# Kernel tuning notes

Hardware: AMD Instinct MI355X
Metric: run time of the kernel (lower is better)

## Reference

```python
import jax, jax.numpy as jnp
import numpy as np
from jax import lax


def setup_inputs() -> dict:
    key = jax.random.key(0)
    k1, k2 = jax.random.split(key)
    x = jax.random.normal(k1, (16, 256, 64, 64), dtype=jnp.float32)
    weight = jax.random.normal(k2, (1024, 256), dtype=jnp.float32)  # codebook (K, C)
    return {"x": x, "weight": weight}


def reference(x, weight):
    B, C, H, W = x.shape
    # (b c h w) -> (b h w) c
    xf = jnp.transpose(x, (0, 2, 3, 1)).reshape(-1, C)  # [N, C]
    d = (jnp.sum(xf * xf, axis=1, keepdims=True)
         + jnp.sum(weight * weight, axis=1)
         - 2.0 * (xf @ weight.T))
    indices = jnp.argmin(d, axis=1)  # [N], int
    z = weight[indices]  # [N, C] embedding lookup
    codebook_loss = jnp.mean((z - lax.stop_gradient(xf)) ** 2)
    commitment_loss = jnp.mean((xf - lax.stop_gradient(z)) ** 2)
    # straight-through estimator
    zq = xf + lax.stop_gradient(z - xf)
    zq = zq.reshape(B, H, W, C).transpose(0, 3, 1, 2)  # back to [B, C, H, W]
    sequence = indices.reshape(B, H, W)
    return zq, sequence, codebook_loss, commitment_loss
```

## Files before the change

kernel.cpp:

```cpp
#include <hip/hip_runtime.h>
#include <cfloat>

#define B_   16
#define C_   256
#define K_   1024
#define HW_  4096
#define N_   (B_ * HW_)
#define CHW_ (C_ * HW_)

#define SEQ_OFF  (B_ * C_ * HW_)
#define LOSS_OFF (SEQ_OFF + N_)

#define WT_F    0
#define WN_F    262144
#define WHB_F   263168
#define WLB_F   394240
#define RLIST_F 525312
#define RCNT_F  590848

#define EPS_GAP 0.03125f

typedef short bf16x8 __attribute__((ext_vector_type(8)));
typedef float f32x16 __attribute__((ext_vector_type(16)));

__device__ __forceinline__ unsigned short bf16_rne(float f) {
    unsigned u = __float_as_uint(f);
    unsigned r = u + 0x7fffu + ((u >> 16) & 1u);
    return (unsigned short)(r >> 16);
}
__device__ __forceinline__ float bf16_to_f(unsigned short h) {
    return __uint_as_float(((unsigned)h) << 16);
}

__global__ __launch_bounds__(256) void transpose_w_kernel(
    const float* __restrict__ w, float* __restrict__ w_t)
{
    const int tid = blockIdx.x * 256 + threadIdx.x;
    const float4 v = reinterpret_cast<const float4*>(w)[tid];
    const int k = tid >> 6;
    const int c = (tid & 63) * 4;
    w_t[(size_t)(c + 0) * K_ + k] = v.x;
    w_t[(size_t)(c + 1) * K_ + k] = v.y;
    w_t[(size_t)(c + 2) * K_ + k] = v.z;
    w_t[(size_t)(c + 3) * K_ + k] = v.w;
}

__global__ __launch_bounds__(256) void wnorm_kernel(
    const float* __restrict__ w, float* __restrict__ wn)
{
    const int k = blockIdx.x * 256 + threadIdx.x;
    const float4* wr = reinterpret_cast<const float4*>(w + (size_t)k * C_);
    float s = 0.f;
#pragma unroll 8
    for (int c4 = 0; c4 < C_ / 4; ++c4) {
        const float4 v = wr[c4];
        s += v.x * v.x + v.y * v.y + v.z * v.z + v.w * v.w;
    }
    wn[k] = s;
}

__global__ __launch_bounds__(256) void wsplit_frag_kernel(
    const float* __restrict__ w, unsigned short* __restrict__ whb,
    unsigned short* __restrict__ wlb)
{
    const int tid = blockIdx.x * 256 + threadIdx.x;
    const int k  = tid >> 5;
    const int c8 = tid & 31;
    const float* src = w + (size_t)k * C_ + c8 * 8;
    unsigned short h[8], lo[8];
#pragma unroll
    for (int j = 0; j < 8; ++j) {
        const float v = src[j];
        h[j] = bf16_rne(v);
        lo[j] = bf16_rne(v - bf16_to_f(h[j]));
    }
    const size_t dst = (size_t)(k >> 5) * 8192 + (size_t)c8 * 256 + (size_t)(k & 31) * 8;
#pragma unroll
    for (int j = 0; j < 8; ++j) { whb[dst + j] = h[j]; wlb[dst + j] = lo[j]; }
}

__global__ __launch_bounds__(256, 2) void argmin_mfma_kernel(
    const float* __restrict__ x, const unsigned short* __restrict__ whb,
    const unsigned short* __restrict__ wlb, const float* __restrict__ wnorm,
    float* __restrict__ seq, int* __restrict__ rlist, int* __restrict__ rcount)
{
    __shared__ __align__(16) char lds[65536];
    const int t  = threadIdx.x;
    const int l  = t & 63;
    const int wv = t >> 6;
    const int nb = blockIdx.x;
    const int b  = nb >> 5;
    const int hw0 = (nb & 31) << 7;
    const float* xb = x + (size_t)b * CHW_ + hw0;

    const int col   = l & 31;
    const int khalf = l >> 5;

    bf16x8 ah[16], al[16];
    {
        float* xs = (float*)lds;
#pragma unroll
        for (int cc = 0; cc < 8; ++cc) {
#pragma unroll
            for (int q = 0; q < 4; ++q) {
                const int fi = q * 256 + t;
                const int cl = fi >> 5;
                const int r4 = (fi & 31) << 2;
                const float4 v = *reinterpret_cast<const float4*>(
                    xb + (size_t)(cc * 32 + cl) * HW_ + r4);
                *reinterpret_cast<float4*>(xs + cl * 132 + r4) = v;
            }
            __syncthreads();
            const int row = wv * 32 + col;
#pragma unroll
            for (int h = 0; h < 2; ++h) {
                const int ks = cc * 2 + h;
                bf16x8 vh, vl;
#pragma unroll
                for (int j = 0; j < 8; ++j) {
                    const float v = xs[(h * 16 + khalf * 8 + j) * 132 + row];
                    const unsigned short hi = bf16_rne(v);
                    vh[j] = (short)hi;
                    vl[j] = (short)bf16_rne(v - bf16_to_f(hi));
                }
                ah[ks] = vh;
                al[ks] = vl;
            }
            __syncthreads();
        }
    }

    char* const buf0 = lds;
    char* const buf1 = lds + 32768;
    const char* whbB = (const char*)whb;
    const char* wlbB = (const char*)wlb;

#define STAGE_CHUNK(ch, dst)                                                        \
    {                                                                               \
        const size_t goff = (size_t)(ch) * 16384 + (size_t)(wv * 4) * 1024;         \
        const int    loff = wv * 4 * 1024;                                          \
        _Pragma("unroll")                                                           \
        for (int rr = 0; rr < 4; ++rr) {                                            \
            __builtin_amdgcn_global_load_lds(                                       \
                (const __attribute__((address_space(1))) void*)                    \
                    (whbB + goff + rr * 1024 + l * 16),                             \
                (__attribute__((address_space(3))) void*)                           \
                    ((dst) + loff + rr * 1024), 16, 0, 0);                          \
            __builtin_amdgcn_global_load_lds(                                       \
                (const __attribute__((address_space(1))) void*)                    \
                    (wlbB + goff + rr * 1024 + l * 16),                             \
                (__attribute__((address_space(3))) void*)                           \
                    ((dst) + 16384 + loff + rr * 1024), 16, 0, 0);                  \
        }                                                                           \
    }

    STAGE_CHUNK(0, buf0);
    __syncthreads();

    float m1v[16], m2v[16];
    int   i1v[16];
#pragma unroll
    for (int r = 0; r < 16; ++r) { m1v[r] = FLT_MAX; m2v[r] = FLT_MAX; i1v[r] = 0; }

    for (int ch = 0; ch < 32; ++ch) {
        char* const curbuf = (ch & 1) ? buf1 : buf0;
        if (ch < 31) { STAGE_CHUNK(ch + 1, (ch & 1) ? buf0 : buf1); }
        const int k0 = ch * 32;
        const float wnc = wnorm[k0 + col];

        f32x16 accA = {0.f}, accB = {0.f};
#pragma unroll
        for (int r = 0; r < 16; ++r) { accA[r] = 0.f; accB[r] = 0.f; }

        const char* hb = curbuf;
        const char* lb = curbuf + 16384;
#pragma unroll
        for (int ks = 0; ks < 16; ++ks) {
            const bf16x8 bh = *reinterpret_cast<const bf16x8*>(hb + ks * 1024 + (l << 4));
            const bf16x8 bl = *reinterpret_cast<const bf16x8*>(lb + ks * 1024 + (l << 4));
            accA = __builtin_amdgcn_mfma_f32_32x32x16_bf16(ah[ks], bh, accA, 0, 0, 0);
            accB = __builtin_amdgcn_mfma_f32_32x32x16_bf16(al[ks], bh, accB, 0, 0, 0);
            accA = __builtin_amdgcn_mfma_f32_32x32x16_bf16(ah[ks], bl, accA, 0, 0, 0);
        }

        const int kidx = k0 + col;
#pragma unroll
        for (int r = 0; r < 16; ++r) {
            const float d = fmaf(-2.f, accA[r] + accB[r], wnc);
            const bool lt = d < m1v[r];
            m2v[r] = lt ? m1v[r] : fminf(m2v[r], d);
            i1v[r] = lt ? kidx : i1v[r];
            m1v[r] = lt ? d : m1v[r];
        }
        __syncthreads();
    }
#undef STAGE_CHUNK

#pragma unroll
    for (int mask = 1; mask <= 16; mask <<= 1) {
#pragma unroll
        for (int r = 0; r < 16; ++r) {
            const float om1 = __shfl_xor(m1v[r], mask, 64);
            const int   oi1 = __shfl_xor(i1v[r], mask, 64);
            const float om2 = __shfl_xor(m2v[r], mask, 64);
            const bool lt = om1 < m1v[r] || (om1 == m1v[r] && oi1 < i1v[r]);
            const float nm2 = lt ? fminf(m1v[r], om2) : fminf(m2v[r], om1);
            i1v[r] = lt ? oi1 : i1v[r];
            m1v[r] = lt ? om1 : m1v[r];
            m2v[r] = nm2;
        }
    }

    if (col == 0) {
#pragma unroll
        for (int r = 0; r < 16; ++r) {
            const int row_local = (r & 3) + 8 * (r >> 2) + 4 * khalf;
            const int n = b * HW_ + hw0 + wv * 32 + row_local;
            seq[n] = (float)i1v[r];
            if (m2v[r] - m1v[r] < EPS_GAP) {
                const int pos = atomicAdd(rcount, 1);
                rlist[pos] = n;
            }
        }
    }
}

__global__ __launch_bounds__(256) void rescue_kernel(
    const float* __restrict__ x, const float* __restrict__ w_t,
    const float* __restrict__ wnorm, const int* __restrict__ rlist,
    const int* __restrict__ rcount, float* __restrict__ seq)
{
    __shared__ float xr[C_];
    __shared__ float bvs[4];
    __shared__ int   bis[4];
    const int t = threadIdx.x;
    const int cnt = *rcount;
    for (int ii = blockIdx.x; ii < cnt; ii += gridDim.x) {
        const int n = rlist[ii];
        const int b = n >> 12, hw = n & 4095;
        xr[t] = x[(size_t)b * CHW_ + (size_t)t * HW_ + hw];
        __syncthreads();
        float best = FLT_MAX; int bidx = 0;
#pragma unroll
        for (int q = 0; q < 4; ++q) {
            const int k = t + q * 256;
            float acc = 0.f;
            for (int c = 0; c < C_; ++c) acc = fmaf(xr[c], w_t[(size_t)c * K_ + k], acc);
            const float d = wnorm[k] - 2.f * acc;
            if (d < best || (d == best && k < bidx)) { best = d; bidx = k; }
        }
#pragma unroll
        for (int mask = 1; mask < 64; mask <<= 1) {
            const float ov = __shfl_xor(best, mask, 64);
            const int   oi = __shfl_xor(bidx, mask, 64);
            if (ov < best || (ov == best && oi < bidx)) { best = ov; bidx = oi; }
        }
        if ((t & 63) == 0) { bvs[t >> 6] = best; bis[t >> 6] = bidx; }
        __syncthreads();
        if (t == 0) {
            float bv = bvs[0]; int bi = bis[0];
#pragma unroll
            for (int w2 = 1; w2 < 4; ++w2)
                if (bvs[w2] < bv || (bvs[w2] == bv && bis[w2] < bi)) { bv = bvs[w2]; bi = bis[w2]; }
            seq[n] = (float)bi;
        }
        __syncthreads();
    }
}

__global__ __launch_bounds__(256) void gather_kernel(
    const float* __restrict__ x, const float* __restrict__ w,
    const float* __restrict__ seqf, float* __restrict__ zq,
    double* __restrict__ loss_acc)
{
    const int t   = threadIdx.x;
    const int nb  = blockIdx.x;
    const int b   = nb >> 6;
    const int hw0 = (nb & 63) << 6;
    const int r   = t & 63;
    const int cg  = t >> 6;
    const float* xb = x  + (size_t)b * CHW_ + hw0;
    float*       zb = zq + (size_t)b * CHW_ + hw0;
    const int idx = (int)seqf[b * HW_ + hw0 + r];
    const float* wrow = w + (size_t)idx * C_;

    float lsum = 0.f;
#pragma unroll 4
    for (int cc = 0; cc < 64; ++cc) {
        const int c = cg * 64 + cc;
        const float xv = xb[(size_t)c * HW_ + r];
        const float d  = wrow[c] - xv;
        zb[(size_t)c * HW_ + r] = xv + d;
        lsum += d * d;
    }
#pragma unroll
    for (int off = 32; off >= 1; off >>= 1) lsum += __shfl_down(lsum, off, 64);
    __shared__ float wsum[4];
    if ((t & 63) == 0) wsum[t >> 6] = lsum;
    __syncthreads();
    if (t == 0)
        atomicAdd(loss_acc, (double)(wsum[0] + wsum[1] + wsum[2] + wsum[3]));
}

__global__ void finalize_kernel(const double* __restrict__ acc, float* __restrict__ loss_out)
{
    const double s = *acc;
    const float m = (float)(s / (double)((size_t)N_ * C_));
    loss_out[0] = m;
    loss_out[1] = m;
}

extern "C" void kernel_launch(void* const* d_in, const int* in_sizes, int n_in,
                              void* d_out, int out_size, void* d_ws, size_t ws_size,
                              hipStream_t stream)
{
    (void)in_sizes; (void)n_in; (void)out_size; (void)d_ws; (void)ws_size;
    const float* x = (const float*)d_in[0];
    const float* w = (const float*)d_in[1];
    float* out = (float*)d_out;

    float*          w_t    = out + WT_F;
    float*          wn     = out + WN_F;
    unsigned short* whb    = (unsigned short*)(out + WHB_F);
    unsigned short* wlb    = (unsigned short*)(out + WLB_F);
    int*            rlist  = (int*)(out + RLIST_F);
    int*            rcount = (int*)(out + RCNT_F);
    float*          seq    = out + SEQ_OFF;
    double*         loss_acc = (double*)(out + LOSS_OFF);

    transpose_w_kernel<<<256, 256, 0, stream>>>(w, w_t);
    wnorm_kernel<<<4, 256, 0, stream>>>(w, wn);
    wsplit_frag_kernel<<<128, 256, 0, stream>>>(w, whb, wlb);
    hipMemsetAsync((void*)rcount, 0, 4, stream);
    argmin_mfma_kernel<<<512, 256, 0, stream>>>(x, whb, wlb, wn, seq, rlist, rcount);
    rescue_kernel<<<1024, 256, 0, stream>>>(x, w_t, wn, rlist, rcount, seq);
    hipMemsetAsync((char*)d_out + (size_t)LOSS_OFF * 4, 0, 8, stream);
    gather_kernel<<<1024, 256, 0, stream>>>(x, w, seq, out, loss_acc);
    finalize_kernel<<<1, 1, 0, stream>>>(loss_acc, out + LOSS_OFF);
}
```

Measured before the change: 195.0 us.

## Switch argmin distance GEMM from split-bf16 to split-int8 MFMA with K-split waves

```diff
diff --git a/kernel.cpp b/kernel.cpp
--- a/kernel.cpp
+++ b/kernel.cpp
@@ -8,28 +8,25 @@
 #define N_   (B_ * HW_)
 #define CHW_ (C_ * HW_)
 
-#define SEQ_OFF  (B_ * C_ * HW_)
+#define SEQ_OFF  16777216
 #define LOSS_OFF (SEQ_OFF + N_)
-
 #define WT_F    0
 #define WN_F    262144
-#define WHB_F   263168
-#define WLB_F   394240
-#define RLIST_F 525312
-#define RCNT_F  590848
-
-#define EPS_GAP 0.03125f
-
-typedef short bf16x8 __attribute__((ext_vector_type(8)));
-typedef float f32x16 __attribute__((ext_vector_type(16)));
-
-__device__ __forceinline__ unsigned short bf16_rne(float f) {
-    unsigned u = __float_as_uint(f);
-    unsigned r = u + 0x7fffu + ((u >> 16) & 1u);
-    return (unsigned short)(r >> 16);
-}
-__device__ __forceinline__ float bf16_to_f(unsigned short h) {
-    return __uint_as_float(((unsigned)h) << 16);
+#define Q1_F    263168
+#define WQ_F    264192
+#define RLIST_F 395264
+#define RCNT_F  526336
+
+#define EPS_GAP 0.1f
+#define XSCL    20.0f
+#define XINV    0.05f
+#define XOVF    6.3f
+
+typedef int i32x4  __attribute__((ext_vector_type(4)));
+typedef int i32x16 __attribute__((ext_vector_type(16)));
+
+__device__ __forceinline__ int pack4b(int b0, int b1, int b2, int b3) {
+    return (b0 & 0xFF) | ((b1 & 0xFF) << 8) | ((b2 & 0xFF) << 16) | ((b3 & 0xFF) << 24);
 }
 
 __global__ __launch_bounds__(256) void transpose_w_kernel(
@@ -45,156 +42,159 @@
     w_t[(size_t)(c + 3) * K_ + k] = v.w;
 }
 
-__global__ __launch_bounds__(256) void wnorm_kernel(
-    const float* __restrict__ w, float* __restrict__ wn)
-{
-    const int k = blockIdx.x * 256 + threadIdx.x;
-    const float4* wr = reinterpret_cast<const float4*>(w + (size_t)k * C_);
-    float s = 0.f;
-#pragma unroll 8
-    for (int c4 = 0; c4 < C_ / 4; ++c4) {
-        const float4 v = wr[c4];
-        s += v.x * v.x + v.y * v.y + v.z * v.z + v.w * v.w;
-    }
-    wn[k] = s;
-}
-
-__global__ __launch_bounds__(256) void wsplit_frag_kernel(
-    const float* __restrict__ w, unsigned short* __restrict__ whb,
-    unsigned short* __restrict__ wlb)
-{
-    const int tid = blockIdx.x * 256 + threadIdx.x;
-    const int k  = tid >> 5;
-    const int c8 = tid & 31;
-    const float* src = w + (size_t)k * C_ + c8 * 8;
-    unsigned short h[8], lo[8];
-#pragma unroll
-    for (int j = 0; j < 8; ++j) {
-        const float v = src[j];
-        h[j] = bf16_rne(v);
-        lo[j] = bf16_rne(v - bf16_to_f(h[j]));
-    }
-    const size_t dst = (size_t)(k >> 5) * 8192 + (size_t)c8 * 256 + (size_t)(k & 31) * 8;
-#pragma unroll
-    for (int j = 0; j < 8; ++j) { whb[dst + j] = h[j]; wlb[dst + j] = lo[j]; }
-}
-
-__global__ __launch_bounds__(256, 2) void argmin_mfma_kernel(
-    const float* __restrict__ x, const unsigned short* __restrict__ whb,
-    const unsigned short* __restrict__ wlb, const float* __restrict__ wnorm,
+__global__ __launch_bounds__(256) void wprep_kernel(
+    const float* __restrict__ w, unsigned char* __restrict__ wq,
+    float* __restrict__ wn, float* __restrict__ q1)
+{
+    const int t = threadIdx.x;
+    const int l = t & 63;
+    const int k = blockIdx.x * 4 + (t >> 6);
+    const float4 v4 = *reinterpret_cast<const float4*>(w + (size_t)k * C_ + l * 4);
+    float vv[4] = {v4.x, v4.y, v4.z, v4.w};
+    float mx = fmaxf(fmaxf(fabsf(vv[0]), fabsf(vv[1])), fmaxf(fabsf(vv[2]), fabsf(vv[3])));
+    float s2 = vv[0]*vv[0] + vv[1]*vv[1] + vv[2]*vv[2] + vv[3]*vv[3];
+#pragma unroll
+    for (int m = 1; m < 64; m <<= 1) {
+        mx = fmaxf(mx, __shfl_xor(mx, m, 64));
+        s2 += __shfl_xor(s2, m, 64);
+    }
+    const float s  = 127.4f / fmaxf(mx, 1e-20f);
+    const float d1 = 1.0f / s;
+    const float sl = s * 256.0f;
+    const int chunk = k >> 5;
+    const int col   = k & 31;
+#pragma unroll
+    for (int q = 0; q < 4; ++q) {
+        const int c = l * 4 + q;
+        const float v = vv[q];
+        const int qh = (int)rintf(v * s);
+        const float r = fmaf((float)qh, -d1, v);
+        int ql = (int)rintf(r * sl);
+        ql = max(-127, min(127, ql));
+        const size_t off = (size_t)chunk * 16384 + (size_t)(c >> 5) * 1024
+                         + (size_t)((c >> 4) & 1) * 512 + (size_t)col * 16 + (size_t)(c & 15);
+        wq[off]        = (unsigned char)(qh & 0xFF);
+        wq[off + 8192] = (unsigned char)(ql & 0xFF);
+    }
+    if (l == 0) { wn[k] = s2; q1[k] = 0.1f * d1; }
+}
+
+__global__ __launch_bounds__(512, 4) void argmin_i8_kernel(
+    const float* __restrict__ x, const unsigned char* __restrict__ wq,
+    const float* __restrict__ wn, const float* __restrict__ q1,
     float* __restrict__ seq, int* __restrict__ rlist, int* __restrict__ rcount)
 {
     __shared__ __align__(16) char lds[65536];
     const int t  = threadIdx.x;
     const int l  = t & 63;
     const int wv = t >> 6;
+    const int mg = wv & 3;
+    const int g2 = wv >> 2;
+    const int col = l & 31;
+    const int khalf = l >> 5;
     const int nb = blockIdx.x;
     const int b  = nb >> 5;
     const int hw0 = (nb & 31) << 7;
     const float* xb = x + (size_t)b * CHW_ + hw0;
 
-    const int col   = l & 31;
-    const int khalf = l >> 5;
-
-    bf16x8 ah[16], al[16];
+    char* const buf0 = lds;
+    char* const buf1 = lds + 32768;
+
+#define STAGE64(ch, dst)                                                          \
+    {                                                                             \
+        _Pragma("unroll")                                                         \
+        for (int rr = 0; rr < 4; ++rr) {                                          \
+            const int sIdx = wv * 4 + rr;                                         \
+            __builtin_amdgcn_global_load_lds(                                     \
+                (const __attribute__((address_space(1))) void*)                   \
+                    (wq + (size_t)(ch) * 32768 + sIdx * 1024 + l * 16),           \
+                (__attribute__((address_space(3))) void*)((dst) + sIdx * 1024),   \
+                16, 0, 0);                                                        \
+        }                                                                         \
+    }
+
+    STAGE64(0, buf1);
+
+    i32x4 ah8[8], al8[8];
+    float mx = 0.f;
     {
-        float* xs = (float*)lds;
+        float* xs = (float*)buf0;
 #pragma unroll
         for (int cc = 0; cc < 8; ++cc) {
 #pragma unroll
-            for (int q = 0; q < 4; ++q) {
-                const int fi = q * 256 + t;
+            for (int qq = 0; qq < 2; ++qq) {
+                const int fi = qq * 512 + t;
                 const int cl = fi >> 5;
                 const int r4 = (fi & 31) << 2;
                 const float4 v = *reinterpret_cast<const float4*>(
                     xb + (size_t)(cc * 32 + cl) * HW_ + r4);
-                *reinterpret_cast<float4*>(xs + cl * 132 + r4) = v;
+                *reinterpret_cast<float4*>(xs + cl * 128 + r4) = v;
             }
             __syncthreads();
-            const int row = wv * 32 + col;
-#pragma unroll
-            for (int h = 0; h < 2; ++h) {
-                const int ks = cc * 2 + h;
-                bf16x8 vh, vl;
-#pragma unroll
-                for (int j = 0; j < 8; ++j) {
-                    const float v = xs[(h * 16 + khalf * 8 + j) * 132 + row];
-                    const unsigned short hi = bf16_rne(v);
-                    vh[j] = (short)hi;
-                    vl[j] = (short)bf16_rne(v - bf16_to_f(hi));
-                }
-                ah[ks] = vh;
-                al[ks] = vl;
+            const int row = mg * 32 + col;
+            int qh[16], ql[16];
+#pragma unroll
+            for (int j = 0; j < 16; ++j) {
+                const float v = xs[(khalf * 16 + j) * 128 + row];
+                mx = fmaxf(mx, fabsf(v));
+                const int h = (int)rintf(v * XSCL);
+                const float r = fmaf((float)h, -XINV, v);
+                int lo = (int)rintf(r * (XSCL * 256.0f));
+                lo = max(-127, min(127, lo));
+                qh[j] = h; ql[j] = lo;
             }
+            ah8[cc] = (i32x4){ pack4b(qh[0],qh[1],qh[2],qh[3]),   pack4b(qh[4],qh[5],qh[6],qh[7]),
+                               pack4b(qh[8],qh[9],qh[10],qh[11]), pack4b(qh[12],qh[13],qh[14],qh[15]) };
+            al8[cc] = (i32x4){ pack4b(ql[0],ql[1],ql[2],ql[3]),   pack4b(ql[4],ql[5],ql[6],ql[7]),
+                               pack4b(ql[8],ql[9],ql[10],ql[11]), pack4b(ql[12],ql[13],ql[14],ql[15]) };
             __syncthreads();
         }
     }
 
-    char* const buf0 = lds;
-    char* const buf1 = lds + 32768;
-    const char* whbB = (const char*)whb;
-    const char* wlbB = (const char*)wlb;
-
-#define STAGE_CHUNK(ch, dst)                                                        \
-    {                                                                               \
-        const size_t goff = (size_t)(ch) * 16384 + (size_t)(wv * 4) * 1024;         \
-        const int    loff = wv * 4 * 1024;                                          \
-        _Pragma("unroll")                                                           \
-        for (int rr = 0; rr < 4; ++rr) {                                            \
-            __builtin_amdgcn_global_load_lds(                                       \
-                (const __attribute__((address_space(1))) void*)                    \
-                    (whbB + goff + rr * 1024 + l * 16),                             \
-                (__attribute__((address_space(3))) void*)                           \
-                    ((dst) + loff + rr * 1024), 16, 0, 0);                          \
-            __builtin_amdgcn_global_load_lds(                                       \
-                (const __attribute__((address_space(1))) void*)                    \
-                    (wlbB + goff + rr * 1024 + l * 16),                             \
-                (__attribute__((address_space(3))) void*)                           \
-                    ((dst) + 16384 + loff + rr * 1024), 16, 0, 0);                  \
-        }                                                                           \
-    }
-
-    STAGE_CHUNK(0, buf0);
-    __syncthreads();
+    mx = fmaxf(mx, __shfl_xor(mx, 32, 64));
+    if (wv < 4 && l < 32 && mx > XOVF) {
+        const int pos = atomicAdd(rcount, 1);
+        rlist[pos] = b * HW_ + hw0 + mg * 32 + l;
+    }
 
     float m1v[16], m2v[16];
     int   i1v[16];
 #pragma unroll
     for (int r = 0; r < 16; ++r) { m1v[r] = FLT_MAX; m2v[r] = FLT_MAX; i1v[r] = 0; }
 
-    for (int ch = 0; ch < 32; ++ch) {
-        char* const curbuf = (ch & 1) ? buf1 : buf0;
-        if (ch < 31) { STAGE_CHUNK(ch + 1, (ch & 1) ? buf0 : buf1); }
-        const int k0 = ch * 32;
-        const float wnc = wnorm[k0 + col];
-
-        f32x16 accA = {0.f}, accB = {0.f};
-#pragma unroll
-        for (int r = 0; r < 16; ++r) { accA[r] = 0.f; accB[r] = 0.f; }
-
-        const char* hb = curbuf;
-        const char* lb = curbuf + 16384;
-#pragma unroll
-        for (int ks = 0; ks < 16; ++ks) {
-            const bf16x8 bh = *reinterpret_cast<const bf16x8*>(hb + ks * 1024 + (l << 4));
-            const bf16x8 bl = *reinterpret_cast<const bf16x8*>(lb + ks * 1024 + (l << 4));
-            accA = __builtin_amdgcn_mfma_f32_32x32x16_bf16(ah[ks], bh, accA, 0, 0, 0);
-            accB = __builtin_amdgcn_mfma_f32_32x32x16_bf16(al[ks], bh, accB, 0, 0, 0);
-            accA = __builtin_amdgcn_mfma_f32_32x32x16_bf16(ah[ks], bl, accA, 0, 0, 0);
-        }
-
-        const int kidx = k0 + col;
+    for (int ch = 0; ch < 16; ++ch) {
+        char* const curbuf = (ch & 1) ? buf0 : buf1;
+        if (ch < 15) STAGE64(ch + 1, (ch & 1) ? buf1 : buf0);
+        const int kk = ch * 64 + g2 * 32 + col;
+        const float wnv = wn[kk];
+        const float q1v = q1[kk];
+
+        i32x16 aH, aX;
+#pragma unroll
+        for (int r = 0; r < 16; ++r) { aH[r] = 0; aX[r] = 0; }
+
+        const char* base = curbuf + g2 * 16384;
+#pragma unroll
+        for (int ks = 0; ks < 8; ++ks) {
+            const i32x4 bh = *reinterpret_cast<const i32x4*>(base + ks * 1024 + (l << 4));
+            const i32x4 bl = *reinterpret_cast<const i32x4*>(base + 8192 + ks * 1024 + (l << 4));
+            aH = __builtin_amdgcn_mfma_i32_32x32x32_i8(ah8[ks], bh, aH, 0, 0, 0);
+            aX = __builtin_amdgcn_mfma_i32_32x32x32_i8(ah8[ks], bl, aX, 0, 0, 0);
+            aX = __builtin_amdgcn_mfma_i32_32x32x32_i8(al8[ks], bh, aX, 0, 0, 0);
+        }
+
 #pragma unroll
         for (int r = 0; r < 16; ++r) {
-            const float d = fmaf(-2.f, accA[r] + accB[r], wnc);
+            const float tt = fmaf((float)aX[r], 0.00390625f, (float)aH[r]);
+            const float d  = fmaf(-q1v, tt, wnv);
             const bool lt = d < m1v[r];
             m2v[r] = lt ? m1v[r] : fminf(m2v[r], d);
-            i1v[r] = lt ? kidx : i1v[r];
+            i1v[r] = lt ? kk : i1v[r];
             m1v[r] = lt ? d : m1v[r];
         }
         __syncthreads();
     }
-#undef STAGE_CHUNK
+#undef STAGE64
 
 #pragma unroll
     for (int mask = 1; mask <= 16; mask <<= 1) {
@@ -211,13 +211,31 @@
         }
     }
 
-    if (col == 0) {
+    __syncthreads();
+    float* fm1 = (float*)lds;
+    float* fm2 = fm1 + 128;
+    int*   fi1 = (int*)(fm2 + 128);
+    if (wv >= 4 && col == 0) {
 #pragma unroll
         for (int r = 0; r < 16; ++r) {
+            const int idx = mg * 32 + khalf * 16 + r;
+            fm1[idx] = m1v[r]; fm2[idx] = m2v[r]; fi1[idx] = i1v[r];
+        }
+    }
+    __syncthreads();
+    if (wv < 4 && col == 0) {
+#pragma unroll
+        for (int r = 0; r < 16; ++r) {
+            const int idx = mg * 32 + khalf * 16 + r;
+            const float om1 = fm1[idx]; const float om2 = fm2[idx]; const int oi1 = fi1[idx];
+            const bool lt = om1 < m1v[r] || (om1 == m1v[r] && oi1 < i1v[r]);
+            const float nm2 = lt ? fminf(m1v[r], om2) : fminf(m2v[r], om1);
+            const int   ni1 = lt ? oi1 : i1v[r];
+            const float nm1 = lt ? om1 : m1v[r];
             const int row_local = (r & 3) + 8 * (r >> 2) + 4 * khalf;
-            const int n = b * HW_ + hw0 + wv * 32 + row_local;
-            seq[n] = (float)i1v[r];
-            if (m2v[r] - m1v[r] < EPS_GAP) {
+            const int n = b * HW_ + hw0 + mg * 32 + row_local;
+            seq[n] = (float)ni1;
+            if (nm2 - nm1 < EPS_GAP) {
                 const int pos = atomicAdd(rcount, 1);
                 rlist[pos] = n;
             }
@@ -273,33 +291,46 @@
     const float* __restrict__ seqf, float* __restrict__ zq,
     double* __restrict__ loss_acc)
 {
+    __shared__ float ws[C_ * 64];
     const int t   = threadIdx.x;
     const int nb  = blockIdx.x;
     const int b   = nb >> 6;
     const int hw0 = (nb & 63) << 6;
-    const int r   = t & 63;
-    const int cg  = t >> 6;
+    {
+        const int j = t >> 2, q = t & 3;
+        const int idx = (int)seqf[b * HW_ + hw0 + j];
+        const float* wrow = w + (size_t)idx * C_ + q * 64;
+#pragma unroll
+        for (int m = 0; m < 16; ++m) {
+            const float4 v = *reinterpret_cast<const float4*>(wrow + m * 4);
+            const int c = q * 64 + m * 4;
+            ws[(c + 0) * 64 + j] = v.x;
+            ws[(c + 1) * 64 + j] = v.y;
+            ws[(c + 2) * 64 + j] = v.z;
+            ws[(c + 3) * 64 + j] = v.w;
+        }
+    }
+    __syncthreads();
+    const int r  = t & 63;
+    const int cg = t >> 6;
     const float* xb = x  + (size_t)b * CHW_ + hw0;
     float*       zb = zq + (size_t)b * CHW_ + hw0;
-    const int idx = (int)seqf[b * HW_ + hw0 + r];
-    const float* wrow = w + (size_t)idx * C_;
-
     float lsum = 0.f;
 #pragma unroll 4
     for (int cc = 0; cc < 64; ++cc) {
         const int c = cg * 64 + cc;
         const float xv = xb[(size_t)c * HW_ + r];
-        const float d  = wrow[c] - xv;
+        const float d  = ws[c * 64 + r] - xv;
         zb[(size_t)c * HW_ + r] = xv + d;
         lsum += d * d;
     }
 #pragma unroll
     for (int off = 32; off >= 1; off >>= 1) lsum += __shfl_down(lsum, off, 64);
-    __shared__ float wsum[4];
-    if ((t & 63) == 0) wsum[t >> 6] = lsum;
+    __syncthreads();
+    if ((t & 63) == 0) ws[t >> 6] = lsum;
     __syncthreads();
     if (t == 0)
-        atomicAdd(loss_acc, (double)(wsum[0] + wsum[1] + wsum[2] + wsum[3]));
+        atomicAdd(loss_acc, (double)(ws[0] + ws[1] + ws[2] + ws[3]));
 }
 
 __global__ void finalize_kernel(const double* __restrict__ acc, float* __restrict__ loss_out)
@@ -319,20 +350,19 @@
     const float* w = (const float*)d_in[1];
     float* out = (float*)d_out;
 
-    float*          w_t    = out + WT_F;
-    float*          wn     = out + WN_F;
-    unsigned short* whb    = (unsigned short*)(out + WHB_F);
-    unsigned short* wlb    = (unsigned short*)(out + WLB_F);
-    int*            rlist  = (int*)(out + RLIST_F);
-    int*            rcount = (int*)(out + RCNT_F);
-    float*          seq    = out + SEQ_OFF;
-    double*         loss_acc = (double*)(out + LOSS_OFF);
+    float*         w_t    = out + WT_F;
+    float*         wn     = out + WN_F;
+    float*         q1     = out + Q1_F;
+    unsigned char* wq     = (unsigned char*)(out + WQ_F);
+    int*           rlist  = (int*)(out + RLIST_F);
+    int*           rcount = (int*)(out + RCNT_F);
+    float*         seq    = out + SEQ_OFF;
+    double*        loss_acc = (double*)(out + LOSS_OFF);
 
     transpose_w_kernel<<<256, 256, 0, stream>>>(w, w_t);
-    wnorm_kernel<<<4, 256, 0, stream>>>(w, wn);
-    wsplit_frag_kernel<<<128, 256, 0, stream>>>(w, whb, wlb);
+    wprep_kernel<<<256, 256, 0, stream>>>(w, wq, wn, q1);
     hipMemsetAsync((void*)rcount, 0, 4, stream);
-    argmin_mfma_kernel<<<512, 256, 0, stream>>>(x, whb, wlb, wn, seq, rlist, rcount);
+    argmin_i8_kernel<<<512, 512, 0, stream>>>(x, wq, wn, q1, seq, rlist, rcount);
     rescue_kernel<<<1024, 256, 0, stream>>>(x, w_t, wn, rlist, rcount, seq);
     hipMemsetAsync((char*)d_out + (size_t)LOSS_OFF * 4, 0, 8, stream);
     gather_kernel<<<1024, 256, 0, stream>>>(x, w, seq, out, loss_acc);
```

After: 311.3 us. 59.6% more time.
